# Kernel optimization log

Measured on AMD Instinct MI355X. Metric: run time of the kernel, lower is better.

Reference implementation:

```python
import jax, jax.numpy as jnp
import numpy as np

N_EXPERTS = 64
TOP_K = 8
ALPHA = 0.01
EMBED_DIM = 2048


def setup_inputs() -> dict:
    key = jax.random.key(0)
    k1, k2 = jax.random.split(key)
    hidden_states = jax.random.normal(k1, (4, 8192, EMBED_DIM), dtype=jnp.float32)
    # router weight, torch init-style scale
    weight = jax.random.normal(k2, (N_EXPERTS, EMBED_DIM), dtype=jnp.float32) / np.sqrt(EMBED_DIM)
    return {"hidden_states": hidden_states, "weight": weight}


def reference(hidden_states, weight):
    # flatten tokens: [B,S,D] -> [N,D]
    x = hidden_states.reshape(-1, hidden_states.shape[-1])
    # router logits: [N,E]
    logits = jnp.einsum('nd,ed->ne', x, weight)
    scores = jax.nn.softmax(logits, axis=-1)
    # top-k routing weights and expert ids (torch uses sorted=False; order is immaterial)
    topk_weight, topk_idx = jax.lax.top_k(scores, TOP_K)
    # aux load-balance loss (training path, alpha > 0)
    counts = jnp.bincount(topk_idx.reshape(-1), length=N_EXPERTS).astype(scores.dtype)
    ce = counts / topk_idx.size  # fraction of assignments per expert
    Pi = scores.mean(axis=0)     # mean router prob per expert
    aux_loss = jnp.sum(Pi * ce * N_EXPERTS) * ALPHA
    return topk_idx, topk_weight, aux_loss
```

## Files before the change

kernel.cpp:

```cpp
#include <hip/hip_runtime.h>

#define EMBED_D  2048
#define N_EXP    64
#define K_TOP    8
#define TOK_BLK  64
#define THREADS  256
#define NCHUNK   64
#define WCHUNK_B 12288
#define XCHUNK_B 8192
#define BUF_B    (WCHUNK_B + XCHUNK_B)
#define NBUF     3

typedef __attribute__((ext_vector_type(8))) short bf16x8;
typedef __attribute__((ext_vector_type(4))) float f32x4;

__device__ __forceinline__ uint bf16_rne(float x) {
    uint u = __float_as_uint(x);
    return (u + 0x7fffu + ((u >> 16) & 1u)) >> 16;
}
__device__ __forceinline__ float bf16f(uint h) { return __uint_as_float(h << 16); }

__device__ __forceinline__ void stage16(const void* g, void* l)
{
    typedef __attribute__((address_space(1))) const unsigned int gu32;
    typedef __attribute__((address_space(3))) unsigned int lu32;
    __builtin_amdgcn_global_load_lds((gu32*)g, (lu32*)l, 16, 0, 0);
}

__device__ __forceinline__ void split3(float4 u, float4 v, bf16x8& H, bf16x8& M, bf16x8& L)
{
    const float x[8] = {u.x, u.y, u.z, u.w, v.x, v.y, v.z, v.w};
    uint hw[8], mw[8], lw[8];
#pragma unroll
    for (int j = 0; j < 8; ++j) {
        const uint ux = __float_as_uint(x[j]);
        hw[j] = (ux + 0x7fffu + ((ux >> 16) & 1u)) & 0xffff0000u;
        const float r1 = x[j] - __uint_as_float(hw[j]);
        const uint ur = __float_as_uint(r1);
        mw[j] = (ur + 0x7fffu + ((ur >> 16) & 1u)) & 0xffff0000u;
        lw[j] = __float_as_uint(r1 - __uint_as_float(mw[j]));
    }
    uint* hp = (uint*)&H; uint* mp = (uint*)&M; uint* lp = (uint*)&L;
#pragma unroll
    for (int w = 0; w < 4; ++w) {
        hp[w] = __builtin_amdgcn_perm(hw[2 * w + 1], hw[2 * w], 0x07060302u);
        mp[w] = __builtin_amdgcn_perm(mw[2 * w + 1], mw[2 * w], 0x07060302u);
        lp[w] = __builtin_amdgcn_perm(lw[2 * w + 1], lw[2 * w], 0x07060302u);
    }
}

__global__ void w_prep(const float* __restrict__ W, ushort* __restrict__ WF)
{
    const int e = blockIdx.x;
    const int t = threadIdx.x;
    const float4 a = *(const float4*)(W + (size_t)e * EMBED_D + t * 8);
    const float4 b = *(const float4*)(W + (size_t)e * EMBED_D + t * 8 + 4);
    const float ev[8] = {a.x, a.y, a.z, a.w, b.x, b.y, b.z, b.w};
    ushort h[8], m[8], l[8];
#pragma unroll
    for (int j = 0; j < 8; ++j) {
        const uint hh = bf16_rne(ev[j]);
        const float r1 = ev[j] - bf16f(hh);
        const uint mm = bf16_rne(r1);
        const uint ll = bf16_rne(r1 - bf16f(mm));
        h[j] = (ushort)hh; m[j] = (ushort)mm; l[j] = (ushort)ll;
    }
    const int c = t >> 2;
    const int g = t & 3;
    const int lane = g * 16 + (e & 15);
    const int n    = e >> 4;
    const size_t base = (size_t)c * 6144 + (size_t)n * 512 + (size_t)lane * 8;
    ushort4* H = (ushort4*)(WF + base);
    ushort4* M = (ushort4*)(WF + base + 2048);
    ushort4* L = (ushort4*)(WF + base + 4096);
    H[0] = make_ushort4(h[0], h[1], h[2], h[3]); H[1] = make_ushort4(h[4], h[5], h[6], h[7]);
    M[0] = make_ushort4(m[0], m[1], m[2], m[3]); M[1] = make_ushort4(m[4], m[5], m[6], m[7]);
    L[0] = make_ushort4(l[0], l[1], l[2], l[3]); L[1] = make_ushort4(l[4], l[5], l[6], l[7]);
}

__global__ __launch_bounds__(THREADS, 2) void moe_gate_main(
    const float*  __restrict__ X,
    const ushort* __restrict__ WF,
    float* __restrict__ out,
    float* __restrict__ ws,
    int n_tok)
{
    __shared__ __align__(16) char smem[NBUF * BUF_B];
    __shared__ float sInvZ[TOK_BLK];
    __shared__ float sCnt[N_EXP];
    __shared__ float sColp[4][N_EXP];

    const int tid  = threadIdx.x;
    const int lane = tid & 63;
    const int wv   = __builtin_amdgcn_readfirstlane(tid >> 6);
    const int row  = lane & 15;
    const int g    = lane >> 4;
    const int t0   = blockIdx.x * TOK_BLK;

    const char* wsrc = (const char*)WF + (size_t)(wv * 1024) + lane * 16;
    const float* xsrc[2];
    {
#pragma unroll
        for (int i = 0; i < 2; ++i) {
            const int s  = i * 64 + lane;
            const int lt = s >> 1;
            const int r  = (s & 1) ^ ((lt >> 2) & 1);
            const int gg = lt >> 4, rr = lt & 15;
            xsrc[i] = X + (size_t)(t0 + wv * 16 + rr) * EMBED_D + gg * 8 + r * 4;
        }
    }
    const int c0  = (lane >> 2) & 1;
    const int xo0 = (2 * lane + c0) * 16;
    const int xo1 = (2 * lane + (c0 ^ 1)) * 16;

    f32x4 acc[4];
#pragma unroll
    for (int n = 0; n < 4; ++n) acc[n] = (f32x4){0.f, 0.f, 0.f, 0.f};

#pragma unroll
    for (int c = 0; c < 2; ++c) {
        char* bb = smem + c * BUF_B;
#pragma unroll
        for (int r = 0; r < 3; ++r)
            stage16(wsrc + (size_t)c * WCHUNK_B + r * 4096, bb + (r * 4 + wv) * 1024);
#pragma unroll
        for (int i = 0; i < 2; ++i)
            stage16(xsrc[i] + c * 32, bb + WCHUNK_B + wv * 2048 + i * 1024);
    }

    for (int c = 0; c < NCHUNK; ++c) {
        if (c + 1 < NCHUNK) asm volatile("s_waitcnt vmcnt(5)" ::: "memory");
        else                asm volatile("s_waitcnt vmcnt(0)" ::: "memory");
        __builtin_amdgcn_sched_barrier(0);
        __builtin_amdgcn_s_barrier();

        if (c + 2 < NCHUNK) {
            char* bb = smem + ((c + 2) % NBUF) * BUF_B;
#pragma unroll
            for (int r = 0; r < 3; ++r)
                stage16(wsrc + (size_t)(c + 2) * WCHUNK_B + r * 4096, bb + (r * 4 + wv) * 1024);
#pragma unroll
            for (int i = 0; i < 2; ++i)
                stage16(xsrc[i] + (c + 2) * 32, bb + WCHUNK_B + wv * 2048 + i * 1024);
        }

        const char* bb = smem + (c % NBUF) * BUF_B;
        const char* xb = bb + WCHUNK_B + wv * 2048;

        bf16x8 ah, am, al;
        {
            const float4 u = *(const float4*)(xb + xo0);
            const float4 v = *(const float4*)(xb + xo1);
            split3(u, v, ah, am, al);
        }
#pragma unroll
        for (int n = 0; n < 4; ++n) {
            const char* bp = bb + n * 1024 + lane * 16;
            const bf16x8 bh = *(const bf16x8*)(bp);
            const bf16x8 bm = *(const bf16x8*)(bp + 4096);
            const bf16x8 bl = *(const bf16x8*)(bp + 8192);
            acc[n] = __builtin_amdgcn_mfma_f32_16x16x32_bf16(ah, bh, acc[n], 0, 0, 0);
            acc[n] = __builtin_amdgcn_mfma_f32_16x16x32_bf16(am, bh, acc[n], 0, 0, 0);
            acc[n] = __builtin_amdgcn_mfma_f32_16x16x32_bf16(ah, bm, acc[n], 0, 0, 0);
            acc[n] = __builtin_amdgcn_mfma_f32_16x16x32_bf16(al, bh, acc[n], 0, 0, 0);
            acc[n] = __builtin_amdgcn_mfma_f32_16x16x32_bf16(ah, bl, acc[n], 0, 0, 0);
            acc[n] = __builtin_amdgcn_mfma_f32_16x16x32_bf16(am, bm, acc[n], 0, 0, 0);
        }
    }
    __syncthreads();

    float (*Lp)[N_EXP + 1] = (float (*)[N_EXP + 1])smem;
#pragma unroll
    for (int n = 0; n < 4; ++n)
#pragma unroll
        for (int r = 0; r < 4; ++r)
            Lp[wv * 16 + g * 4 + r][n * 16 + row] = acc[n][r];
    if (tid < N_EXP) sCnt[tid] = 0.f;
    __syncthreads();

    if (tid < TOK_BLK) {
        const int t = tid;
        float mx = -1e30f;
        for (int e = 0; e < N_EXP; ++e)
            mx = fmaxf(mx, Lp[t][e]);
        float Z = 0.f;
        float tv[K_TOP]; int ti[K_TOP];
#pragma unroll
        for (int j = 0; j < K_TOP; ++j) { tv[j] = -1e30f; ti[j] = 0; }
        for (int e = 0; e < N_EXP; ++e) {
            const float s = __expf(Lp[t][e] - mx);
            Lp[t][e] = s;
            Z += s;
            float v = s; int id = e;
#pragma unroll
            for (int j = 0; j < K_TOP; ++j) {
                if (v > tv[j]) {
                    float fv = tv[j]; tv[j] = v; v = fv;
                    int   fi = ti[j]; ti[j] = id; id = fi;
                }
            }
        }
        const float invZ = 1.0f / Z;
        sInvZ[t] = invZ;
        const size_t ob = (size_t)(t0 + t) * K_TOP;
        const size_t wo = (size_t)n_tok * K_TOP;
#pragma unroll
        for (int j = 0; j < K_TOP; ++j) {
            out[ob + j]      = (float)ti[j];
            out[wo + ob + j] = tv[j] * invZ;
            atomicAdd(&sCnt[ti[j]], 1.0f);
        }
    }
    __syncthreads();

    {
        const int e = tid & 63, g2 = tid >> 6;
        float s = 0.f;
#pragma unroll
        for (int i = 0; i < 16; ++i) {
            const int t = g2 * 16 + i;
            s += Lp[t][e] * sInvZ[t];
        }
        sColp[g2][e] = s;
    }
    __syncthreads();
    if (tid < N_EXP) {
        float s = 0.f;
#pragma unroll
        for (int g2 = 0; g2 < 4; ++g2) s += sColp[g2][tid];
        atomicAdd(&ws[64 + tid], s);
        atomicAdd(&ws[tid], sCnt[tid]);
    }
}

__global__ void moe_aux(const float* __restrict__ ws, float* __restrict__ out, int n_tok)
{
    const int e = threadIdx.x;
    const float counts = ws[e];
    const float ssum   = ws[64 + e];
    const float Pi = ssum / (float)n_tok;
    const float ce = counts / ((float)n_tok * (float)K_TOP);
    float term = Pi * ce * (float)N_EXP;
    for (int off = 32; off; off >>= 1) term += __shfl_down(term, off);
    if (e == 0) out[(size_t)2 * n_tok * K_TOP] = term * 0.01f;
}

extern "C" void kernel_launch(void* const* d_in, const int* in_sizes, int n_in,
                              void* d_out, int out_size, void* d_ws, size_t ws_size,
                              hipStream_t stream)
{
    const float* X = (const float*)d_in[0];
    const float* W = (const float*)d_in[1];
    float* out = (float*)d_out;
    float* ws  = (float*)d_ws;
    const int n_tok = in_sizes[0] / EMBED_D;

    ushort* WF = (ushort*)(ws + 256);

    hipMemsetAsync(ws, 0, 2 * N_EXP * sizeof(float), stream);
    w_prep<<<N_EXP, 256, 0, stream>>>(W, WF);
    moe_gate_main<<<n_tok / TOK_BLK, THREADS, 0, stream>>>(X, WF, out, ws, n_tok);
    moe_aux<<<1, 64, 0, stream>>>(ws, out, n_tok);
}
```

Baseline: 421.7 us.

## Load X directly to registers, double token block, stage only weights in LDS

The kernel now handles 128 tokens with 512 threads per block, so each staged weight chunk is shared by twice as many tokens. The fp32 activations are loaded straight from global memory into registers with a two-deep register double buffer, instead of going through LDS via global_load_lds. Only the split bf16 weights are pipelined through a triple-buffered LDS ring, with 64-wide K chunks and a manually unrolled loop body. This cuts LDS traffic and barrier count per K step, in exchange for more register pressure and fewer resident blocks per CU.

```diff
diff --git a/kernel.cpp b/kernel.cpp
--- a/kernel.cpp
+++ b/kernel.cpp
@@ -3,12 +3,10 @@
 #define EMBED_D  2048
 #define N_EXP    64
 #define K_TOP    8
-#define TOK_BLK  64
-#define THREADS  256
-#define NCHUNK   64
-#define WCHUNK_B 12288
-#define XCHUNK_B 8192
-#define BUF_B    (WCHUNK_B + XCHUNK_B)
+#define TOK_BLK  128
+#define THREADS  512
+#define NCHUNK   32
+#define WCHUNK_B 24576
 #define NBUF     3
 
 typedef __attribute__((ext_vector_type(8))) short bf16x8;
@@ -85,10 +83,10 @@
     float* __restrict__ ws,
     int n_tok)
 {
-    __shared__ __align__(16) char smem[NBUF * BUF_B];
+    __shared__ __align__(16) char smem[NBUF * WCHUNK_B];
     __shared__ float sInvZ[TOK_BLK];
     __shared__ float sCnt[N_EXP];
-    __shared__ float sColp[4][N_EXP];
+    __shared__ float sColp[8][N_EXP];
 
     const int tid  = threadIdx.x;
     const int lane = tid & 63;
@@ -97,76 +95,85 @@
     const int g    = lane >> 4;
     const int t0   = blockIdx.x * TOK_BLK;
 
+    const float* xbase = X + (size_t)(t0 + wv * 16 + row) * EMBED_D + (g << 3);
     const char* wsrc = (const char*)WF + (size_t)(wv * 1024) + lane * 16;
-    const float* xsrc[2];
-    {
-#pragma unroll
-        for (int i = 0; i < 2; ++i) {
-            const int s  = i * 64 + lane;
-            const int lt = s >> 1;
-            const int r  = (s & 1) ^ ((lt >> 2) & 1);
-            const int gg = lt >> 4, rr = lt & 15;
-            xsrc[i] = X + (size_t)(t0 + wv * 16 + rr) * EMBED_D + gg * 8 + r * 4;
-        }
-    }
-    const int c0  = (lane >> 2) & 1;
-    const int xo0 = (2 * lane + c0) * 16;
-    const int xo1 = (2 * lane + (c0 ^ 1)) * 16;
 
     f32x4 acc[4];
 #pragma unroll
     for (int n = 0; n < 4; ++n) acc[n] = (f32x4){0.f, 0.f, 0.f, 0.f};
 
-#pragma unroll
-    for (int c = 0; c < 2; ++c) {
-        char* bb = smem + c * BUF_B;
-#pragma unroll
-        for (int r = 0; r < 3; ++r)
-            stage16(wsrc + (size_t)c * WCHUNK_B + r * 4096, bb + (r * 4 + wv) * 1024);
-#pragma unroll
-        for (int i = 0; i < 2; ++i)
-            stage16(xsrc[i] + c * 32, bb + WCHUNK_B + wv * 2048 + i * 1024);
-    }
-
-    for (int c = 0; c < NCHUNK; ++c) {
-        if (c + 1 < NCHUNK) asm volatile("s_waitcnt vmcnt(5)" ::: "memory");
-        else                asm volatile("s_waitcnt vmcnt(0)" ::: "memory");
-        __builtin_amdgcn_sched_barrier(0);
-        __builtin_amdgcn_s_barrier();
-
-        if (c + 2 < NCHUNK) {
-            char* bb = smem + ((c + 2) % NBUF) * BUF_B;
-#pragma unroll
-            for (int r = 0; r < 3; ++r)
-                stage16(wsrc + (size_t)(c + 2) * WCHUNK_B + r * 4096, bb + (r * 4 + wv) * 1024);
-#pragma unroll
-            for (int i = 0; i < 2; ++i)
-                stage16(xsrc[i] + (c + 2) * 32, bb + WCHUNK_B + wv * 2048 + i * 1024);
-        }
-
-        const char* bb = smem + (c % NBUF) * BUF_B;
-        const char* xb = bb + WCHUNK_B + wv * 2048;
-
-        bf16x8 ah, am, al;
-        {
-            const float4 u = *(const float4*)(xb + xo0);
-            const float4 v = *(const float4*)(xb + xo1);
-            split3(u, v, ah, am, al);
-        }
-#pragma unroll
-        for (int n = 0; n < 4; ++n) {
-            const char* bp = bb + n * 1024 + lane * 16;
-            const bf16x8 bh = *(const bf16x8*)(bp);
-            const bf16x8 bm = *(const bf16x8*)(bp + 4096);
-            const bf16x8 bl = *(const bf16x8*)(bp + 8192);
-            acc[n] = __builtin_amdgcn_mfma_f32_16x16x32_bf16(ah, bh, acc[n], 0, 0, 0);
-            acc[n] = __builtin_amdgcn_mfma_f32_16x16x32_bf16(am, bh, acc[n], 0, 0, 0);
-            acc[n] = __builtin_amdgcn_mfma_f32_16x16x32_bf16(ah, bm, acc[n], 0, 0, 0);
-            acc[n] = __builtin_amdgcn_mfma_f32_16x16x32_bf16(al, bh, acc[n], 0, 0, 0);
-            acc[n] = __builtin_amdgcn_mfma_f32_16x16x32_bf16(ah, bl, acc[n], 0, 0, 0);
-            acc[n] = __builtin_amdgcn_mfma_f32_16x16x32_bf16(am, bm, acc[n], 0, 0, 0);
-        }
-    }
+    float4 xA[4], xB[4];
+
+    xA[0] = *(const float4*)(xbase);
+    xA[1] = *(const float4*)(xbase + 4);
+    xA[2] = *(const float4*)(xbase + 32);
+    xA[3] = *(const float4*)(xbase + 36);
+#pragma unroll
+    for (int r = 0; r < 3; ++r)
+        stage16(wsrc + r * 8192, smem + wv * 1024 + r * 8192);
+    __builtin_amdgcn_sched_barrier(0);
+    xB[0] = *(const float4*)(xbase + 64);
+    xB[1] = *(const float4*)(xbase + 68);
+    xB[2] = *(const float4*)(xbase + 96);
+    xB[3] = *(const float4*)(xbase + 100);
+#pragma unroll
+    for (int r = 0; r < 3; ++r)
+        stage16(wsrc + WCHUNK_B + r * 8192, smem + WCHUNK_B + wv * 1024 + r * 8192);
+    __builtin_amdgcn_sched_barrier(0);
+
+    int s_cur = 0;
+
+#define BODY(C, XQ)                                                              \
+    {                                                                            \
+        __builtin_amdgcn_sched_barrier(0);                                       \
+        if ((C) + 1 < NCHUNK) asm volatile("s_waitcnt vmcnt(7)" ::: "memory");   \
+        else                  asm volatile("s_waitcnt vmcnt(0)" ::: "memory");   \
+        __builtin_amdgcn_sched_barrier(0);                                       \
+        __builtin_amdgcn_s_barrier();                                            \
+        __builtin_amdgcn_sched_barrier(0);                                       \
+        const char* bb = smem + s_cur * WCHUNK_B;                                \
+        _Pragma("unroll")                                                        \
+        for (int kk = 0; kk < 2; ++kk) {                                         \
+            bf16x8 ah, am, al;                                                   \
+            split3(XQ[2 * kk], XQ[2 * kk + 1], ah, am, al);                      \
+            _Pragma("unroll")                                                    \
+            for (int n = 0; n < 4; ++n) {                                        \
+                const char* bp = bb + kk * 12288 + n * 1024 + (lane << 4);       \
+                const bf16x8 bh = *(const bf16x8*)(bp);                          \
+                const bf16x8 bm = *(const bf16x8*)(bp + 4096);                   \
+                const bf16x8 bl = *(const bf16x8*)(bp + 8192);                   \
+                acc[n] = __builtin_amdgcn_mfma_f32_16x16x32_bf16(ah, bh, acc[n], 0, 0, 0); \
+                acc[n] = __builtin_amdgcn_mfma_f32_16x16x32_bf16(am, bh, acc[n], 0, 0, 0); \
+                acc[n] = __builtin_amdgcn_mfma_f32_16x16x32_bf16(ah, bm, acc[n], 0, 0, 0); \
+                acc[n] = __builtin_amdgcn_mfma_f32_16x16x32_bf16(al, bh, acc[n], 0, 0, 0); \
+                acc[n] = __builtin_amdgcn_mfma_f32_16x16x32_bf16(ah, bl, acc[n], 0, 0, 0); \
+                acc[n] = __builtin_amdgcn_mfma_f32_16x16x32_bf16(am, bm, acc[n], 0, 0, 0); \
+            }                                                                    \
+        }                                                                        \
+        __builtin_amdgcn_sched_barrier(0);                                       \
+        if ((C) + 2 < NCHUNK) {                                                  \
+            const float* xs = xbase + ((C) + 2) * 64;                            \
+            XQ[0] = *(const float4*)(xs);                                        \
+            XQ[1] = *(const float4*)(xs + 4);                                    \
+            XQ[2] = *(const float4*)(xs + 32);                                   \
+            XQ[3] = *(const float4*)(xs + 36);                                   \
+            const int s2 = (s_cur + 2 >= NBUF) ? s_cur - 1 : s_cur + 2;          \
+            char* db = smem + s2 * WCHUNK_B + wv * 1024;                         \
+            const char* gw = wsrc + (size_t)((C) + 2) * WCHUNK_B;                \
+            stage16(gw,         db);                                             \
+            stage16(gw + 8192,  db + 8192);                                      \
+            stage16(gw + 16384, db + 16384);                                     \
+        }                                                                        \
+        __builtin_amdgcn_sched_barrier(0);                                       \
+        s_cur = (s_cur == NBUF - 1) ? 0 : s_cur + 1;                             \
+    }
+
+    for (int c = 0; c < NCHUNK; c += 2) {
+        BODY(c, xA)
+        BODY(c + 1, xB)
+    }
+#undef BODY
+
     __syncthreads();
 
     float (*Lp)[N_EXP + 1] = (float (*)[N_EXP + 1])smem;
@@ -227,7 +234,7 @@
     if (tid < N_EXP) {
         float s = 0.f;
 #pragma unroll
-        for (int g2 = 0; g2 < 4; ++g2) s += sColp[g2][tid];
+        for (int g2 = 0; g2 < 8; ++g2) s += sColp[g2][tid];
         atomicAdd(&ws[64 + tid], s);
         atomicAdd(&ws[tid], sCnt[tid]);
     }
```

Measured after the change: 411.3 us. 2.5% less time.

## Halve token tile, split waves across experts, load X straight to registers

Applied to the files above, without the earlier changes.

Token block size drops from 64 to 32. The four waves are now arranged as 2 token groups by 2 expert halves, so each wave holds two accumulators instead of four. X tiles are no longer staged through LDS; they are loaded directly into registers and software-prefetched two chunks ahead. The launch bound rises to 4 blocks per CU, which shrinks LDS use and register pressure so occupancy and the number of blocks both double. The cost is that the split weight matrix is re-read by twice as many blocks, adding L2 traffic.

```diff
diff --git a/kernel.cpp b/kernel.cpp
--- a/kernel.cpp
+++ b/kernel.cpp
@@ -3,12 +3,10 @@
 #define EMBED_D  2048
 #define N_EXP    64
 #define K_TOP    8
-#define TOK_BLK  64
+#define TOK_BLK  32
 #define THREADS  256
 #define NCHUNK   64
 #define WCHUNK_B 12288
-#define XCHUNK_B 8192
-#define BUF_B    (WCHUNK_B + XCHUNK_B)
 #define NBUF     3
 
 typedef __attribute__((ext_vector_type(8))) short bf16x8;
@@ -78,14 +76,14 @@
     L[0] = make_ushort4(l[0], l[1], l[2], l[3]); L[1] = make_ushort4(l[4], l[5], l[6], l[7]);
 }
 
-__global__ __launch_bounds__(THREADS, 2) void moe_gate_main(
+__global__ __launch_bounds__(THREADS, 4) void moe_gate_main(
     const float*  __restrict__ X,
     const ushort* __restrict__ WF,
     float* __restrict__ out,
     float* __restrict__ ws,
     int n_tok)
 {
-    __shared__ __align__(16) char smem[NBUF * BUF_B];
+    __shared__ __align__(16) char smem[NBUF * WCHUNK_B];
     __shared__ float sInvZ[TOK_BLK];
     __shared__ float sCnt[N_EXP];
     __shared__ float sColp[4][N_EXP];
@@ -93,88 +91,86 @@
     const int tid  = threadIdx.x;
     const int lane = tid & 63;
     const int wv   = __builtin_amdgcn_readfirstlane(tid >> 6);
+    const int tg   = wv >> 1;
+    const int eh   = wv & 1;
     const int row  = lane & 15;
     const int g    = lane >> 4;
     const int t0   = blockIdx.x * TOK_BLK;
 
+    const float* xbase = X + (size_t)(t0 + tg * 16 + row) * EMBED_D + (g << 3);
     const char* wsrc = (const char*)WF + (size_t)(wv * 1024) + lane * 16;
-    const float* xsrc[2];
-    {
-#pragma unroll
-        for (int i = 0; i < 2; ++i) {
-            const int s  = i * 64 + lane;
-            const int lt = s >> 1;
-            const int r  = (s & 1) ^ ((lt >> 2) & 1);
-            const int gg = lt >> 4, rr = lt & 15;
-            xsrc[i] = X + (size_t)(t0 + wv * 16 + rr) * EMBED_D + gg * 8 + r * 4;
-        }
-    }
-    const int c0  = (lane >> 2) & 1;
-    const int xo0 = (2 * lane + c0) * 16;
-    const int xo1 = (2 * lane + (c0 ^ 1)) * 16;
-
-    f32x4 acc[4];
-#pragma unroll
-    for (int n = 0; n < 4; ++n) acc[n] = (f32x4){0.f, 0.f, 0.f, 0.f};
-
-#pragma unroll
-    for (int c = 0; c < 2; ++c) {
-        char* bb = smem + c * BUF_B;
-#pragma unroll
-        for (int r = 0; r < 3; ++r)
-            stage16(wsrc + (size_t)c * WCHUNK_B + r * 4096, bb + (r * 4 + wv) * 1024);
-#pragma unroll
-        for (int i = 0; i < 2; ++i)
-            stage16(xsrc[i] + c * 32, bb + WCHUNK_B + wv * 2048 + i * 1024);
-    }
-
+
+    f32x4 acc[2];
+    acc[0] = (f32x4){0.f, 0.f, 0.f, 0.f};
+    acc[1] = (f32x4){0.f, 0.f, 0.f, 0.f};
+
+    float4 xc0, xc1, xn0, xn1;
+
+    xc0 = *(const float4*)(xbase);
+    xc1 = *(const float4*)(xbase + 4);
+#pragma unroll
+    for (int r = 0; r < 3; ++r)
+        stage16(wsrc + r * 4096, smem + (r * 4 + wv) * 1024);
+    __builtin_amdgcn_sched_barrier(0);
+    xn0 = *(const float4*)(xbase + 32);
+    xn1 = *(const float4*)(xbase + 36);
+#pragma unroll
+    for (int r = 0; r < 3; ++r)
+        stage16(wsrc + WCHUNK_B + r * 4096, smem + WCHUNK_B + (r * 4 + wv) * 1024);
+    __builtin_amdgcn_sched_barrier(0);
+
+    int s_cur = 0;
     for (int c = 0; c < NCHUNK; ++c) {
         if (c + 1 < NCHUNK) asm volatile("s_waitcnt vmcnt(5)" ::: "memory");
         else                asm volatile("s_waitcnt vmcnt(0)" ::: "memory");
         __builtin_amdgcn_sched_barrier(0);
         __builtin_amdgcn_s_barrier();
-
+        __builtin_amdgcn_sched_barrier(0);
+
+        float4 tq0 = {0, 0, 0, 0}, tq1 = {0, 0, 0, 0};
         if (c + 2 < NCHUNK) {
-            char* bb = smem + ((c + 2) % NBUF) * BUF_B;
-#pragma unroll
-            for (int r = 0; r < 3; ++r)
-                stage16(wsrc + (size_t)(c + 2) * WCHUNK_B + r * 4096, bb + (r * 4 + wv) * 1024);
-#pragma unroll
-            for (int i = 0; i < 2; ++i)
-                stage16(xsrc[i] + (c + 2) * 32, bb + WCHUNK_B + wv * 2048 + i * 1024);
-        }
-
-        const char* bb = smem + (c % NBUF) * BUF_B;
-        const char* xb = bb + WCHUNK_B + wv * 2048;
+            const float* xs = xbase + (c + 2) * 32;
+            tq0 = *(const float4*)(xs);
+            tq1 = *(const float4*)(xs + 4);
+            const int s2 = (s_cur >= 1) ? s_cur - 1 : 2;
+            char* db = smem + s2 * WCHUNK_B;
+            const char* gw = wsrc + (size_t)(c + 2) * WCHUNK_B;
+            stage16(gw,        db + (0 * 4 + wv) * 1024);
+            stage16(gw + 4096, db + (1 * 4 + wv) * 1024);
+            stage16(gw + 8192, db + (2 * 4 + wv) * 1024);
+        }
+        __builtin_amdgcn_sched_barrier(0);
 
         bf16x8 ah, am, al;
-        {
-            const float4 u = *(const float4*)(xb + xo0);
-            const float4 v = *(const float4*)(xb + xo1);
-            split3(u, v, ah, am, al);
-        }
-#pragma unroll
-        for (int n = 0; n < 4; ++n) {
-            const char* bp = bb + n * 1024 + lane * 16;
+        split3(xc0, xc1, ah, am, al);
+        const char* bb = smem + s_cur * WCHUNK_B;
+#pragma unroll
+        for (int nl = 0; nl < 2; ++nl) {
+            const int n = eh * 2 + nl;
+            const char* bp = bb + n * 1024 + (lane << 4);
             const bf16x8 bh = *(const bf16x8*)(bp);
             const bf16x8 bm = *(const bf16x8*)(bp + 4096);
             const bf16x8 bl = *(const bf16x8*)(bp + 8192);
-            acc[n] = __builtin_amdgcn_mfma_f32_16x16x32_bf16(ah, bh, acc[n], 0, 0, 0);
-            acc[n] = __builtin_amdgcn_mfma_f32_16x16x32_bf16(am, bh, acc[n], 0, 0, 0);
-            acc[n] = __builtin_amdgcn_mfma_f32_16x16x32_bf16(ah, bm, acc[n], 0, 0, 0);
-            acc[n] = __builtin_amdgcn_mfma_f32_16x16x32_bf16(al, bh, acc[n], 0, 0, 0);
-            acc[n] = __builtin_amdgcn_mfma_f32_16x16x32_bf16(ah, bl, acc[n], 0, 0, 0);
-            acc[n] = __builtin_amdgcn_mfma_f32_16x16x32_bf16(am, bm, acc[n], 0, 0, 0);
-        }
+            acc[nl] = __builtin_amdgcn_mfma_f32_16x16x32_bf16(ah, bh, acc[nl], 0, 0, 0);
+            acc[nl] = __builtin_amdgcn_mfma_f32_16x16x32_bf16(am, bh, acc[nl], 0, 0, 0);
+            acc[nl] = __builtin_amdgcn_mfma_f32_16x16x32_bf16(ah, bm, acc[nl], 0, 0, 0);
+            acc[nl] = __builtin_amdgcn_mfma_f32_16x16x32_bf16(al, bh, acc[nl], 0, 0, 0);
+            acc[nl] = __builtin_amdgcn_mfma_f32_16x16x32_bf16(ah, bl, acc[nl], 0, 0, 0);
+            acc[nl] = __builtin_amdgcn_mfma_f32_16x16x32_bf16(am, bm, acc[nl], 0, 0, 0);
+        }
+        __builtin_amdgcn_sched_barrier(0);
+
+        xc0 = xn0; xc1 = xn1; xn0 = tq0; xn1 = tq1;
+        s_cur = (s_cur == NBUF - 1) ? 0 : s_cur + 1;
     }
     __syncthreads();
 
     float (*Lp)[N_EXP + 1] = (float (*)[N_EXP + 1])smem;
 #pragma unroll
-    for (int n = 0; n < 4; ++n)
+    for (int nl = 0; nl < 2; ++nl)
 #pragma unroll
         for (int r = 0; r < 4; ++r)
-            Lp[wv * 16 + g * 4 + r][n * 16 + row] = acc[n][r];
+            Lp[tg * 16 + g * 4 + r][(eh * 2 + nl) * 16 + row] = acc[nl][r];
     if (tid < N_EXP) sCnt[tid] = 0.f;
     __syncthreads();
 
@@ -217,8 +213,8 @@
         const int e = tid & 63, g2 = tid >> 6;
         float s = 0.f;
 #pragma unroll
-        for (int i = 0; i < 16; ++i) {
-            const int t = g2 * 16 + i;
+        for (int i = 0; i < 8; ++i) {
+            const int t = g2 * 8 + i;
             s += Lp[t][e] * sInvZ[t];
         }
         sColp[g2][e] = s;
```

New measurement: 443.8 us. 5.2% more time.

## Load X chunks directly into registers and deepen weight LDS pipeline to four stages

Applied to the files above, without the earlier changes.

Activation chunks are no longer staged through LDS with global_load_lds. Each lane now loads its own float4 pairs straight into a four-slot register ring, four chunks ahead. Weight chunks keep the LDS path, but the buffer count rises to four with a prefetch distance of three, and the main loop is unrolled by four with hand-tuned vmcnt waits. This aims to cut LDS traffic and reads for X and to hide more global latency. In exchange it uses more registers, which may hurt occupancy, and it relies on exact vmcnt accounting, where any mismatch would be a correctness risk.

```diff
diff --git a/kernel.cpp b/kernel.cpp
--- a/kernel.cpp
+++ b/kernel.cpp
@@ -7,9 +7,7 @@
 #define THREADS  256
 #define NCHUNK   64
 #define WCHUNK_B 12288
-#define XCHUNK_B 8192
-#define BUF_B    (WCHUNK_B + XCHUNK_B)
-#define NBUF     3
+#define NBUF     4
 
 typedef __attribute__((ext_vector_type(8))) short bf16x8;
 typedef __attribute__((ext_vector_type(4))) float f32x4;
@@ -85,7 +83,7 @@
     float* __restrict__ ws,
     int n_tok)
 {
-    __shared__ __align__(16) char smem[NBUF * BUF_B];
+    __shared__ __align__(16) char smem[NBUF * WCHUNK_B];
     __shared__ float sInvZ[TOK_BLK];
     __shared__ float sCnt[N_EXP];
     __shared__ float sColp[4][N_EXP];
@@ -97,76 +95,85 @@
     const int g    = lane >> 4;
     const int t0   = blockIdx.x * TOK_BLK;
 
+    const float* xbase = X + (size_t)(t0 + wv * 16 + row) * EMBED_D + (g << 3);
     const char* wsrc = (const char*)WF + (size_t)(wv * 1024) + lane * 16;
-    const float* xsrc[2];
-    {
-#pragma unroll
-        for (int i = 0; i < 2; ++i) {
-            const int s  = i * 64 + lane;
-            const int lt = s >> 1;
-            const int r  = (s & 1) ^ ((lt >> 2) & 1);
-            const int gg = lt >> 4, rr = lt & 15;
-            xsrc[i] = X + (size_t)(t0 + wv * 16 + rr) * EMBED_D + gg * 8 + r * 4;
-        }
-    }
-    const int c0  = (lane >> 2) & 1;
-    const int xo0 = (2 * lane + c0) * 16;
-    const int xo1 = (2 * lane + (c0 ^ 1)) * 16;
 
     f32x4 acc[4];
 #pragma unroll
     for (int n = 0; n < 4; ++n) acc[n] = (f32x4){0.f, 0.f, 0.f, 0.f};
 
-#pragma unroll
-    for (int c = 0; c < 2; ++c) {
-        char* bb = smem + c * BUF_B;
-#pragma unroll
-        for (int r = 0; r < 3; ++r)
-            stage16(wsrc + (size_t)c * WCHUNK_B + r * 4096, bb + (r * 4 + wv) * 1024);
-#pragma unroll
-        for (int i = 0; i < 2; ++i)
-            stage16(xsrc[i] + c * 32, bb + WCHUNK_B + wv * 2048 + i * 1024);
-    }
-
-    for (int c = 0; c < NCHUNK; ++c) {
-        if (c + 1 < NCHUNK) asm volatile("s_waitcnt vmcnt(5)" ::: "memory");
-        else                asm volatile("s_waitcnt vmcnt(0)" ::: "memory");
-        __builtin_amdgcn_sched_barrier(0);
-        __builtin_amdgcn_s_barrier();
-
-        if (c + 2 < NCHUNK) {
-            char* bb = smem + ((c + 2) % NBUF) * BUF_B;
-#pragma unroll
-            for (int r = 0; r < 3; ++r)
-                stage16(wsrc + (size_t)(c + 2) * WCHUNK_B + r * 4096, bb + (r * 4 + wv) * 1024);
-#pragma unroll
-            for (int i = 0; i < 2; ++i)
-                stage16(xsrc[i] + (c + 2) * 32, bb + WCHUNK_B + wv * 2048 + i * 1024);
-        }
-
-        const char* bb = smem + (c % NBUF) * BUF_B;
-        const char* xb = bb + WCHUNK_B + wv * 2048;
-
-        bf16x8 ah, am, al;
-        {
-            const float4 u = *(const float4*)(xb + xo0);
-            const float4 v = *(const float4*)(xb + xo1);
-            split3(u, v, ah, am, al);
-        }
-#pragma unroll
-        for (int n = 0; n < 4; ++n) {
-            const char* bp = bb + n * 1024 + lane * 16;
-            const bf16x8 bh = *(const bf16x8*)(bp);
-            const bf16x8 bm = *(const bf16x8*)(bp + 4096);
-            const bf16x8 bl = *(const bf16x8*)(bp + 8192);
-            acc[n] = __builtin_amdgcn_mfma_f32_16x16x32_bf16(ah, bh, acc[n], 0, 0, 0);
-            acc[n] = __builtin_amdgcn_mfma_f32_16x16x32_bf16(am, bh, acc[n], 0, 0, 0);
-            acc[n] = __builtin_amdgcn_mfma_f32_16x16x32_bf16(ah, bm, acc[n], 0, 0, 0);
-            acc[n] = __builtin_amdgcn_mfma_f32_16x16x32_bf16(al, bh, acc[n], 0, 0, 0);
-            acc[n] = __builtin_amdgcn_mfma_f32_16x16x32_bf16(ah, bl, acc[n], 0, 0, 0);
-            acc[n] = __builtin_amdgcn_mfma_f32_16x16x32_bf16(am, bm, acc[n], 0, 0, 0);
-        }
-    }
+    float4 xr[4][2];
+
+#define STAGE_W(C, SLOT)                                                        \
+    {                                                                           \
+        const char* gw = wsrc + (size_t)(C) * WCHUNK_B;                         \
+        char* db = smem + (SLOT) * WCHUNK_B;                                    \
+        stage16(gw,        db + (0 * 4 + wv) * 1024);                           \
+        stage16(gw + 4096, db + (1 * 4 + wv) * 1024);                           \
+        stage16(gw + 8192, db + (2 * 4 + wv) * 1024);                           \
+    }
+#define LOAD_X(C, SLOT)                                                         \
+    {                                                                           \
+        const float* xs = xbase + (C) * 32;                                     \
+        xr[SLOT][0] = *(const float4*)(xs);                                     \
+        xr[SLOT][1] = *(const float4*)(xs + 4);                                 \
+    }
+
+    LOAD_X(0, 0)
+    STAGE_W(0, 0)
+    __builtin_amdgcn_sched_barrier(0);
+    LOAD_X(1, 1)
+    STAGE_W(1, 1)
+    __builtin_amdgcn_sched_barrier(0);
+    LOAD_X(2, 2)
+    STAGE_W(2, 2)
+    __builtin_amdgcn_sched_barrier(0);
+    LOAD_X(3, 3)
+    __builtin_amdgcn_sched_barrier(0);
+
+#define BODY(C, U, VM, DO_W, DO_X)                                              \
+    {                                                                           \
+        asm volatile("s_waitcnt vmcnt(" #VM ")" ::: "memory");                  \
+        __builtin_amdgcn_sched_barrier(0);                                      \
+        __builtin_amdgcn_s_barrier();                                           \
+        __builtin_amdgcn_sched_barrier(0);                                      \
+        if (DO_W) STAGE_W((C) + 3, ((U) + 3) & 3)                               \
+        __builtin_amdgcn_sched_barrier(0);                                      \
+        bf16x8 ah, am, al;                                                      \
+        split3(xr[U][0], xr[U][1], ah, am, al);                                 \
+        if (DO_X) LOAD_X((C) + 4, U)                                            \
+        __builtin_amdgcn_sched_barrier(0);                                      \
+        const char* bb = smem + (U) * WCHUNK_B;                                 \
+        _Pragma("unroll")                                                       \
+        for (int n = 0; n < 4; ++n) {                                           \
+            const char* bp = bb + n * 1024 + (lane << 4);                       \
+            const bf16x8 bh = *(const bf16x8*)(bp);                             \
+            const bf16x8 bm = *(const bf16x8*)(bp + 4096);                      \
+            const bf16x8 bl = *(const bf16x8*)(bp + 8192);                      \
+            acc[n] = __builtin_amdgcn_mfma_f32_16x16x32_bf16(ah, bh, acc[n], 0, 0, 0); \
+            acc[n] = __builtin_amdgcn_mfma_f32_16x16x32_bf16(am, bh, acc[n], 0, 0, 0); \
+            acc[n] = __builtin_amdgcn_mfma_f32_16x16x32_bf16(ah, bm, acc[n], 0, 0, 0); \
+            acc[n] = __builtin_amdgcn_mfma_f32_16x16x32_bf16(al, bh, acc[n], 0, 0, 0); \
+            acc[n] = __builtin_amdgcn_mfma_f32_16x16x32_bf16(ah, bl, acc[n], 0, 0, 0); \
+            acc[n] = __builtin_amdgcn_mfma_f32_16x16x32_bf16(am, bm, acc[n], 0, 0, 0); \
+        }                                                                       \
+        __builtin_amdgcn_sched_barrier(0);                                      \
+    }
+
+    for (int cc = 0; cc < NCHUNK - 4; cc += 4) {
+        BODY(cc + 0, 0, 12, 1, 1)
+        BODY(cc + 1, 1, 12, 1, 1)
+        BODY(cc + 2, 2, 12, 1, 1)
+        BODY(cc + 3, 3, 12, 1, 1)
+    }
+    BODY(60, 0, 12, 1, 0)
+    BODY(61, 1, 10, 0, 0)
+    BODY(62, 2, 5, 0, 0)
+    BODY(63, 3, 0, 0, 0)
+#undef BODY
+#undef STAGE_W
+#undef LOAD_X
+
     __syncthreads();
 
     float (*Lp)[N_EXP + 1] = (float (*)[N_EXP + 1])smem;
```

Result: no change. 420.4 us (-0.3%).
